# Optimization experiments

Hardware: AMD Instinct MI355X
Metric: run time of the kernel (lower is better)

The kernel has to match this reference:

```python
import jax, jax.numpy as jnp
import numpy as np

N, K, DIN = 2, 2048, 1024
H, DOUT = 16, 64


def setup_inputs() -> dict:
    key = jax.random.key(0)
    ks = jax.random.split(key, 12)
    c_qk = float(np.sqrt(6.0 / (DIN + DOUT)))  # per-head q/k init scale
    c_v = c_qk  # dim_q == dim_v == DOUT here
    u = lambda k, shape, c: jax.random.uniform(k, shape, jnp.float32, -c, c)
    inp = {
        "query": jax.random.normal(ks[0], (N, K, DIN), jnp.float32),
        "key": jax.random.normal(ks[1], (N, K, DIN), jnp.float32),
        "value": jax.random.normal(ks[2], (N, K, DIN), jnp.float32),
        "mask": jax.random.randint(ks[3], (N, K, K), 0, 2) > 0,  # bool (N,K,K)
        # stacked per-head projection weights: (H, DIN, DOUT), biases (H, DOUT)
        "Wq": u(ks[4], (H, DIN, DOUT), c_qk),
        "bq": u(ks[5], (H, DOUT), c_qk),
        "Wk": u(ks[6], (H, DIN, DOUT), c_qk),
        "bk": u(ks[7], (H, DOUT), c_qk),
        "Wv": u(ks[8], (H, DIN, DOUT), c_v),
        "bv": u(ks[9], (H, DOUT), c_v),
        # output projection: (H*DOUT, DIN)
        "Wp": u(ks[10], (H * DOUT, DIN), c_qk),
        "bp": u(ks[11], (DIN,), c_qk),
    }
    return inp


def reference(query, key, value, mask, Wq, bq, Wk, bk, Wv, bv, Wp, bp):
    # Per-head projections, batched over heads: (N,K,DIN) x (H,DIN,DOUT) -> (N,H,K,DOUT)
    q = jnp.einsum("nkm,hmd->nhkd", query, Wq) + bq[None, :, None, :]
    k = jnp.einsum("nkm,hmd->nhkd", key, Wk) + bk[None, :, None, :]
    v = jnp.einsum("nkm,hmd->nhkd", value, Wv) + bv[None, :, None, :]
    # scaled dot-product scores: (N,H,K,K), scaled by sqrt(per-head dim)
    scores = jnp.einsum("nhkd,nhld->nhkl", q, k) / jnp.sqrt(jnp.asarray(DOUT, q.dtype))
    scores = jnp.where(mask[:, None, :, :], jnp.asarray(-1e9, scores.dtype), scores)
    w = jax.nn.softmax(scores, axis=-1)
    y = jnp.einsum("nhkl,nhld->nhkd", w, v)  # (N,H,K,DOUT)
    # concat heads along feature dim (head order matches torch cat over head list)
    y = jnp.transpose(y, (0, 2, 1, 3)).reshape(N, K, H * DOUT)
    return y @ Wp + bp
```

## Files before the change

### kernel.cpp

```cpp
#include <hip/hip_runtime.h>
#include <hip/hip_bf16.h>
#include <stdint.h>

typedef __attribute__((ext_vector_type(8))) __bf16 bf16x8;
typedef __attribute__((ext_vector_type(2))) __bf16 bf16x2;
typedef __attribute__((ext_vector_type(4))) float floatx4;

#define NB 2
#define SEQ 2048
#define DIN 1024
#define NH 16
#define DH 64
#define DMODEL 1024
#define BQ 128
#define BK 64
#define PAD 72
#define QSCALE 0.18033688011112042f

__device__ __forceinline__ float bf2f(unsigned short u) {
    return __uint_as_float(((unsigned)u) << 16);
}
__device__ __forceinline__ unsigned short f2bf(float f) {
    unsigned u = __float_as_uint(f);
    unsigned r = (u + 0x7FFFu + ((u >> 16) & 1u)) >> 16;
    return (unsigned short)r;
}
__device__ __forceinline__ float ldin(const void* p, size_t idx, int isbf) {
    return isbf ? bf2f(((const unsigned short*)p)[idx]) : ((const float*)p)[idx];
}

__device__ __forceinline__ void gl_lds16(const void* g, void* l) {
    __builtin_amdgcn_global_load_lds(
        reinterpret_cast<__attribute__((address_space(1))) unsigned int*>(
            reinterpret_cast<uintptr_t>(g)),
        reinterpret_cast<__attribute__((address_space(3))) unsigned int*>(
            reinterpret_cast<uintptr_t>(l)),
        16, 0, 0);
}

__device__ __forceinline__ int wave_is_bf16(const void* p) {
    unsigned short u = ((const unsigned short*)p)[2 * (threadIdx.x & 63)];
    int e = (u >> 7) & 0xFF;
    int sane = (u == 0 || (e > 100 && e < 140)) ? 1 : 0;
    return __popcll(__ballot(sane)) >= 32;
}
__device__ __forceinline__ int wave_mask_is_int(const void* p) {
    int v = ((const int*)p)[threadIdx.x & 63];
    int zo = (v == 0 || v == 1) ? 1 : 0;
    return __popcll(__ballot(zo)) >= 48;
}

__global__ __launch_bounds__(256) void prep(
    const void* __restrict__ q, const void* __restrict__ k, const void* __restrict__ v,
    const void* __restrict__ mask,
    const void* __restrict__ wq, const void* __restrict__ wk,
    const void* __restrict__ wv, const void* __restrict__ wp,
    unsigned short* __restrict__ a0, unsigned short* __restrict__ a1,
    unsigned short* __restrict__ a2,
    unsigned short* __restrict__ t0, unsigned short* __restrict__ t1,
    unsigned short* __restrict__ t2, unsigned short* __restrict__ t3,
    unsigned int* __restrict__ mbits)
{
    __shared__ float xls[64][68];
    const int b = blockIdx.x;
    const int tid = threadIdx.x;
    if (b < 12288) {
        int z = b >> 12, blk = b & 4095;
        const void* src = (z == 0) ? q : (z == 1) ? k : v;
        unsigned short* dst = (z == 0) ? a0 : (z == 1) ? a1 : a2;
        int isbf = wave_is_bf16(src);
        size_t i = ((size_t)blk * 256 + tid) * 4;
        if (isbf) {
            *(ushort4*)&dst[i] = *(const ushort4*)((const unsigned short*)src + i);
        } else {
            float4 f = *(const float4*)((const float*)src + i);
            ushort4 o;
            o.x = f2bf(f.x); o.y = f2bf(f.y); o.z = f2bf(f.z); o.w = f2bf(f.w);
            *(ushort4*)&dst[i] = o;
        }
    } else if (b < 13312) {
        int blk = b - 12288;
        int w = blk * 256 + tid;
        int is_int = wave_mask_is_int(mask);
        unsigned bits = 0;
        if (is_int) {
            const int4* p = (const int4*)mask + (size_t)w * 8;
#pragma unroll
            for (int g = 0; g < 8; ++g) {
                int4 vv = p[g];
                bits |= (unsigned)(vv.x != 0) << (g * 4 + 0);
                bits |= (unsigned)(vv.y != 0) << (g * 4 + 1);
                bits |= (unsigned)(vv.z != 0) << (g * 4 + 2);
                bits |= (unsigned)(vv.w != 0) << (g * 4 + 3);
            }
        } else {
            const uint4* p = (const uint4*)mask + (size_t)w * 2;
#pragma unroll
            for (int g = 0; g < 2; ++g) {
                uint4 vv = p[g];
                unsigned ws4[4] = {vv.x, vv.y, vv.z, vv.w};
#pragma unroll
                for (int c = 0; c < 4; ++c)
#pragma unroll
                    for (int bb = 0; bb < 4; ++bb)
                        bits |= (unsigned)(((ws4[c] >> (8 * bb)) & 0xFFu) != 0)
                                << (g * 16 + c * 4 + bb);
            }
        }
        mbits[w] = bits;
    } else {
        int zb = b - 13312;
        int z = zb >> 8, t = zb & 255;
        const void* src = (z == 0) ? wq : (z == 1) ? wk : (z == 2) ? wv : wp;
        unsigned short* dst = (z == 0) ? t0 : (z == 1) ? t1 : (z == 2) ? t2 : t3;
        int isbf = wave_is_bf16(src);
        int r = tid >> 2, cs = (tid & 3) * 16;
        if (z < 3) {
            int h = t >> 4, m0 = (t & 15) * 64;
#pragma unroll
            for (int j = 0; j < 16; ++j)
                xls[r][cs + j] = ldin(src, (size_t)h * 65536 + (size_t)(m0 + r) * 64 + cs + j, isbf);
            __syncthreads();
            int d2 = tid >> 2, ms = (tid & 3) * 16;
            size_t orow = (size_t)(h * 64 + d2) * 1024 + m0 + ms;
#pragma unroll
            for (int g = 0; g < 4; ++g) {
                ushort4 o;
                o.x = f2bf(xls[ms + g * 4 + 0][d2]);
                o.y = f2bf(xls[ms + g * 4 + 1][d2]);
                o.z = f2bf(xls[ms + g * 4 + 2][d2]);
                o.w = f2bf(xls[ms + g * 4 + 3][d2]);
                *(ushort4*)&dst[orow + g * 4] = o;
            }
        } else {
            int m0 = (t >> 4) * 64, c0 = (t & 15) * 64;
#pragma unroll
            for (int j = 0; j < 16; ++j)
                xls[r][cs + j] = ldin(src, (size_t)(m0 + r) * 1024 + c0 + cs + j, isbf);
            __syncthreads();
            int d2 = tid >> 2, ms = (tid & 3) * 16;
            size_t orow = (size_t)(c0 + d2) * 1024 + m0 + ms;
#pragma unroll
            for (int g = 0; g < 4; ++g) {
                ushort4 o;
                o.x = f2bf(xls[ms + g * 4 + 0][d2]);
                o.y = f2bf(xls[ms + g * 4 + 1][d2]);
                o.z = f2bf(xls[ms + g * 4 + 2][d2]);
                o.w = f2bf(xls[ms + g * 4 + 3][d2]);
                *(ushort4*)&dst[orow + g * 4] = o;
            }
        }
    }
}

__global__ __launch_bounds__(256) void gemm_mfma(
    const unsigned short* __restrict__ A0, const unsigned short* __restrict__ A1,
    const unsigned short* __restrict__ A2,
    const unsigned short* __restrict__ B0, const unsigned short* __restrict__ B1,
    const unsigned short* __restrict__ B2,
    const void* __restrict__ bias0, const void* __restrict__ bias1,
    const void* __restrict__ bias2,
    void* __restrict__ C0, void* __restrict__ C1, void* __restrict__ C2,
    int mode0)
{
    const int z = blockIdx.z;
    const unsigned short* A  = (z == 0) ? A0 : (z == 1) ? A1 : A2;
    const unsigned short* BT = (z == 0) ? B0 : (z == 1) ? B1 : B2;
    const void* bias = (z == 0) ? bias0 : (z == 1) ? bias1 : bias2;
    void* C = (z == 0) ? C0 : (z == 1) ? C1 : C2;
    const int mode = mode0 + z;
    const int isbf = wave_is_bf16(bias);
    const float scl = (mode == 0) ? QSCALE : 1.0f;

    const int n0  = blockIdx.x * 128;
    const int m0g = blockIdx.y * 128;
    const int tid = threadIdx.x;
    const int wave = tid >> 6, lane = tid & 63;
    const int l16 = lane & 15, quad = lane >> 4;
    const int wm = wave & 1, wn = wave >> 1;

    __shared__ __align__(16) unsigned short smem[17408];
    unsigned short* As = smem;
    unsigned short* Bs = smem + 8192;

    floatx4 acc[4][4];
#pragma unroll
    for (int mt = 0; mt < 4; ++mt)
#pragma unroll
        for (int nt = 0; nt < 4; ++nt) acc[mt][nt] = floatx4{0.f, 0.f, 0.f, 0.f};

    const int lrow8 = lane >> 3;
    const int lseg  = (lane & 7) * 8;

    for (int kk = 0; kk < 1024; kk += 64) {
#pragma unroll
        for (int j = 0; j < 4; ++j) {
            int row0 = wave * 8 + j * 32;
            gl_lds16(&A[(size_t)(m0g + row0 + lrow8) * 1024 + kk + lseg], &As[row0 * 64]);
            gl_lds16(&BT[(size_t)(n0 + row0 + lrow8) * 1024 + kk + lseg], &Bs[row0 * 64]);
        }
        __syncthreads();
#pragma unroll
        for (int ks = 0; ks < 2; ++ks) {
            bf16x8 af[4], bf[4];
#pragma unroll
            for (int mt = 0; mt < 4; ++mt)
                af[mt] = *(const bf16x8*)&As[(wm * 64 + mt * 16 + l16) * 64 + ks * 32 + quad * 8];
#pragma unroll
            for (int nt = 0; nt < 4; ++nt)
                bf[nt] = *(const bf16x8*)&Bs[(wn * 64 + nt * 16 + l16) * 64 + ks * 32 + quad * 8];
#pragma unroll
            for (int mt = 0; mt < 4; ++mt)
#pragma unroll
                for (int nt = 0; nt < 4; ++nt)
                    acc[mt][nt] = __builtin_amdgcn_mfma_f32_16x16x32_bf16(af[mt], bf[nt], acc[mt][nt], 0, 0, 0);
        }
        __syncthreads();
    }

    float bv4[4];
#pragma unroll
    for (int nt = 0; nt < 4; ++nt)
        bv4[nt] = ldin(bias, n0 + wn * 64 + nt * 16 + l16, isbf);

    if (mode <= 1) {
        unsigned short* O = (unsigned short*)C;
#pragma unroll
        for (int mt = 0; mt < 4; ++mt)
#pragma unroll
            for (int reg = 0; reg < 4; ++reg) {
                int row = m0g + wm * 64 + mt * 16 + quad * 4 + reg;
                int nb = row >> 11, kq = row & (SEQ - 1);
#pragma unroll
                for (int nt = 0; nt < 4; ++nt) {
                    int c = n0 + wn * 64 + nt * 16 + l16;
                    int h = c >> 6, d = c & 63;
                    O[(((size_t)nb * NH + h) * SEQ + kq) * DH + d] =
                        f2bf((acc[mt][nt][reg] + bv4[nt]) * scl);
                }
            }
    } else if (mode == 2) {
#pragma unroll
        for (int mt = 0; mt < 4; ++mt)
#pragma unroll
            for (int nt = 0; nt < 4; ++nt)
#pragma unroll
                for (int reg = 0; reg < 4; ++reg) {
                    int m_l = wm * 64 + mt * 16 + quad * 4 + reg;
                    int c_l = wn * 64 + nt * 16 + l16;
                    smem[c_l * 136 + m_l] = f2bf(acc[mt][nt][reg] + bv4[nt]);
                }
        __syncthreads();
        unsigned short* O = (unsigned short*)C;
        int nb = m0g >> 11;
        int kq0 = m0g & (SEQ - 1);
#pragma unroll
        for (int j = 0; j < 8; ++j) {
            int i = tid + j * 256;
            int c_l = i >> 4, m8 = (i & 15) * 8;
            int cg = n0 + c_l, h = cg >> 6, d = cg & 63;
            *(bf16x8*)&O[(((size_t)nb * NH + h) * DH + d) * SEQ + kq0 + m8] =
                *(const bf16x8*)&smem[c_l * 136 + m8];
        }
    } else {
        unsigned short* Ob = (unsigned short*)C;
        float* Of = (float*)C;
#pragma unroll
        for (int mt = 0; mt < 4; ++mt)
#pragma unroll
            for (int reg = 0; reg < 4; ++reg) {
                int row = m0g + wm * 64 + mt * 16 + quad * 4 + reg;
#pragma unroll
                for (int nt = 0; nt < 4; ++nt) {
                    int c = n0 + wn * 64 + nt * 16 + l16;
                    float v = acc[mt][nt][reg] + bv4[nt];
                    if (isbf) Ob[(size_t)row * DMODEL + c] = f2bf(v);
                    else      Of[(size_t)row * DMODEL + c] = v;
                }
            }
    }
}

__global__ __launch_bounds__(256, 2) void attn_mfma(
    const unsigned short* __restrict__ qws, const unsigned short* __restrict__ kws,
    const unsigned short* __restrict__ vtws, const unsigned int* __restrict__ mbits,
    unsigned short* __restrict__ yws)
{
    const int linear = blockIdx.x + (blockIdx.y << 4) + (blockIdx.z << 8);
    const int xcd = linear & 7, loc = linear >> 3;
    const int hn  = (xcd << 2) + (loc >> 4);
    const int qt  = loc & 15;
    const int h   = hn & 15;
    const int n   = hn >> 4;

    const int tid  = threadIdx.x;
    const int wave = tid >> 6;
    const int lane = tid & 63;
    const int l16  = lane & 15;
    const int quad = lane >> 4;

    __shared__ __align__(16) unsigned short Ks[2][BK * DH];
    __shared__ __align__(16) unsigned short VTs[2][DH * BK];
    __shared__ __align__(16) unsigned short Ps[4][32 * PAD];

    const size_t base_nh = ((size_t)n * NH + h) * SEQ * DH;
    const size_t base_vt = ((size_t)n * NH + h) * DH * SEQ;
    const int q0 = qt * BQ;

    const unsigned int* mr0;
    const unsigned int* mr1;
    bf16x8 af[2][2];
    {
        int qr0 = q0 + wave * 32 + l16;
        int qr1 = qr0 + 16;
        mr0 = mbits + ((size_t)n * SEQ + qr0) * (SEQ / 32);
        mr1 = mbits + ((size_t)n * SEQ + qr1) * (SEQ / 32);
        const unsigned short* qp0 = qws + base_nh + (size_t)qr0 * DH + quad * 8;
        const unsigned short* qp1 = qws + base_nh + (size_t)qr1 * DH + quad * 8;
        af[0][0] = *(const bf16x8*)qp0;
        af[0][1] = *(const bf16x8*)(qp0 + 32);
        af[1][0] = *(const bf16x8*)qp1;
        af[1][1] = *(const bf16x8*)(qp1 + 32);
    }

    const int srow8  = lane >> 3;
    const int schunk = ((lane & 7) ^ srow8) * 8;
    const int swz = l16 & 7;
    int koff[2], voff[2];
#pragma unroll
    for (int ks = 0; ks < 2; ++ks) {
        koff[ks] = l16 * DH + (((ks * 4 + quad) ^ swz) * 8);
        voff[ks] = l16 * BK + (((ks * 4 + quad) ^ swz) * 8);
    }

    bf16x8 vones;
#pragma unroll
    for (int j = 0; j < 8; ++j) vones[j] = (__bf16)1.0f;

#pragma unroll
    for (int j = 0; j < 2; ++j) {
        int rl = wave * 16 + j * 8;
        gl_lds16(&kws[base_nh + (size_t)(rl + srow8) * DH + schunk], &Ks[0][rl * DH]);
        gl_lds16(&vtws[base_vt + (size_t)(rl + srow8) * SEQ + schunk], &VTs[0][rl * BK]);
    }

    floatx4 O[2][4];
#pragma unroll
    for (int g = 0; g < 2; ++g)
#pragma unroll
        for (int dt = 0; dt < 4; ++dt) O[g][dt] = floatx4{0.f, 0.f, 0.f, 0.f};
    floatx4 Lacc[2];
    Lacc[0] = floatx4{0.f, 0.f, 0.f, 0.f};
    Lacc[1] = floatx4{0.f, 0.f, 0.f, 0.f};

    __syncthreads();

    for (int it = 0; it < SEQ / BK; ++it) {
        const int cur = it & 1, nxt = cur ^ 1;
        const bool has_next = (it + 1) < (SEQ / BK);
        const int j0 = it * BK;
        const int j0n = j0 + BK;

        if (has_next) {
#pragma unroll
            for (int j = 0; j < 2; ++j) {
                int rl = wave * 16 + j * 8;
                gl_lds16(&kws[base_nh + (size_t)(j0n + rl + srow8) * DH + schunk], &Ks[nxt][rl * DH]);
                gl_lds16(&vtws[base_vt + (size_t)(rl + srow8) * SEQ + j0n + schunk], &VTs[nxt][rl * BK]);
            }
        }

        uint2 mwA = *(const uint2*)&mr0[j0 >> 5];
        uint2 mwB = *(const uint2*)&mr1[j0 >> 5];

        bf16x8 bfK[4][2];
#pragma unroll
        for (int nt = 0; nt < 4; ++nt)
#pragma unroll
            for (int ks = 0; ks < 2; ++ks)
                bfK[nt][ks] = *(const bf16x8*)&Ks[cur][nt * 16 * DH + koff[ks]];

        float St[2][4][4];
#pragma unroll
        for (int nt = 0; nt < 4; ++nt) {
#pragma unroll
            for (int g = 0; g < 2; ++g) {
                floatx4 c = {0.f, 0.f, 0.f, 0.f};
                c = __builtin_amdgcn_mfma_f32_16x16x32_bf16(bfK[nt][0], af[g][0], c, 0, 0, 0);
                c = __builtin_amdgcn_mfma_f32_16x16x32_bf16(bfK[nt][1], af[g][1], c, 0, 0, 0);
                St[g][nt][0] = c[0]; St[g][nt][1] = c[1];
                St[g][nt][2] = c[2]; St[g][nt][3] = c[3];
            }
        }

#pragma unroll
        for (int g = 0; g < 2; ++g) {
            uint2 mw = g ? mwB : mwA;
#pragma unroll
            for (int nt = 0; nt < 4; ++nt) {
                unsigned w = (nt & 2) ? mw.y : mw.x;
                int bb = (nt & 1) * 16 + quad * 4;
                float p[4];
#pragma unroll
                for (int r = 0; r < 4; ++r) {
                    float e = __builtin_amdgcn_exp2f(St[g][nt][r]);
                    p[r] = ((w >> (bb + r)) & 1u) ? 0.f : e;
                }
                bf16x2 e01, e23;
                e01[0] = (__bf16)p[0]; e01[1] = (__bf16)p[1];
                e23[0] = (__bf16)p[2]; e23[1] = (__bf16)p[3];
                uint2 pk;
                pk.x = *(unsigned*)&e01;
                pk.y = *(unsigned*)&e23;
                *(uint2*)&Ps[wave][(g * 16 + l16) * PAD + nt * 16 + quad * 4] = pk;
            }
        }

        bf16x8 pa[2][2], vb[4][2];
#pragma unroll
        for (int g = 0; g < 2; ++g)
#pragma unroll
            for (int ks = 0; ks < 2; ++ks)
                pa[g][ks] = *(const bf16x8*)&Ps[wave][(g * 16 + l16) * PAD + ks * 32 + quad * 8];
#pragma unroll
        for (int dt = 0; dt < 4; ++dt)
#pragma unroll
            for (int ks = 0; ks < 2; ++ks)
                vb[dt][ks] = *(const bf16x8*)&VTs[cur][dt * 16 * BK + voff[ks]];

        Lacc[0] = __builtin_amdgcn_mfma_f32_16x16x32_bf16(pa[0][0], vones, Lacc[0], 0, 0, 0);
        Lacc[1] = __builtin_amdgcn_mfma_f32_16x16x32_bf16(pa[1][0], vones, Lacc[1], 0, 0, 0);
        Lacc[0] = __builtin_amdgcn_mfma_f32_16x16x32_bf16(pa[0][1], vones, Lacc[0], 0, 0, 0);
        Lacc[1] = __builtin_amdgcn_mfma_f32_16x16x32_bf16(pa[1][1], vones, Lacc[1], 0, 0, 0);
#pragma unroll
        for (int dt = 0; dt < 4; ++dt) {
#pragma unroll
            for (int g = 0; g < 2; ++g) {
                O[g][dt] = __builtin_amdgcn_mfma_f32_16x16x32_bf16(pa[g][0], vb[dt][0], O[g][dt], 0, 0, 0);
                O[g][dt] = __builtin_amdgcn_mfma_f32_16x16x32_bf16(pa[g][1], vb[dt][1], O[g][dt], 0, 0, 0);
            }
        }

        __syncthreads();
    }

#pragma unroll
    for (int g = 0; g < 2; ++g)
#pragma unroll
        for (int r = 0; r < 4; ++r) {
            float lr = Lacc[g][r];
            float inv = (lr > 0.f) ? 1.f / lr : 0.f;
            int row = q0 + wave * 32 + g * 16 + quad * 4 + r;
#pragma unroll
            for (int dt = 0; dt < 4; ++dt) {
                int col = h * DH + dt * 16 + l16;
                yws[((size_t)n * SEQ + row) * DMODEL + col] = f2bf(O[g][dt][r] * inv);
            }
        }
}

extern "C" void kernel_launch(void* const* d_in, const int* in_sizes, int n_in,
                              void* d_out, int out_size, void* d_ws, size_t ws_size,
                              hipStream_t stream) {
    const void* query = d_in[0];
    const void* key_  = d_in[1];
    const void* value = d_in[2];
    const void* mask  = d_in[3];
    const void* Wq = d_in[4];
    const void* bq = d_in[5];
    const void* Wk = d_in[6];
    const void* bk = d_in[7];
    const void* Wv = d_in[8];
    const void* bv = d_in[9];
    const void* Wp = d_in[10];
    const void* bp = d_in[11];

    const size_t per = (size_t)NB * NH * SEQ * DH;
    unsigned short* us = (unsigned short*)d_ws;
    unsigned short* qws  = us;
    unsigned short* kws  = us + per;
    unsigned short* vtws = us + 2 * per;
    unsigned short* abf0 = us + 3 * per;
    unsigned short* abf1 = us + 4 * per;
    unsigned short* abf2 = us + 5 * per;
    unsigned short* wt0  = us + 6 * per;
    unsigned short* wt1  = wt0 + 1048576;
    unsigned short* wt2  = wt1 + 1048576;
    unsigned short* wt3  = wt2 + 1048576;
    unsigned int* mbits  = (unsigned int*)(wt3 + 1048576);
    unsigned short* yws = abf0;

    prep<<<dim3(14336), 256, 0, stream>>>(query, key_, value, mask,
                                          Wq, Wk, Wv, Wp,
                                          abf0, abf1, abf2,
                                          wt0, wt1, wt2, wt3, mbits);
    gemm_mfma<<<dim3(8, 32, 3), 256, 0, stream>>>(abf0, abf1, abf2, wt0, wt1, wt2,
                                                  bq, bk, bv, qws, kws, vtws, 0);
    attn_mfma<<<dim3(SEQ / BQ, NH, NB), 256, 0, stream>>>(qws, kws, vtws, mbits, yws);
    gemm_mfma<<<dim3(8, 32, 1), 256, 0, stream>>>(yws, yws, yws, wt3, wt3, wt3,
                                                  bp, bp, bp, d_out, d_out, d_out, 3);
}
```

Measured before the change: 287.8 us.

## Triple-buffer K/V tiles with partial vmcnt waits and MFMA priority boosts

Replaces the double-buffered K/V LDS pipeline with a three-stage ring that prefetches two tiles ahead, and prefetches the mask words two iterations ahead. The full __syncthreads is replaced by an explicit s_waitcnt vmcnt(6) plus s_barrier, so the current tile's loads must land while the newest prefetch stays in flight. s_setprio is raised around the MFMA blocks to favour matrix issue across waves. This adds LDS usage, which may affect occupancy at 2 blocks/CU, and relies on the hand-counted vmcnt being correct.

```diff
diff --git a/kernel.cpp b/kernel.cpp
--- a/kernel.cpp
+++ b/kernel.cpp
@@ -299,8 +299,8 @@
     const int l16  = lane & 15;
     const int quad = lane >> 4;
 
-    __shared__ __align__(16) unsigned short Ks[2][BK * DH];
-    __shared__ __align__(16) unsigned short VTs[2][DH * BK];
+    __shared__ __align__(16) unsigned short Ks[3][BK * DH];
+    __shared__ __align__(16) unsigned short VTs[3][DH * BK];
     __shared__ __align__(16) unsigned short Ps[4][32 * PAD];
 
     const size_t base_nh = ((size_t)n * NH + h) * SEQ * DH;
@@ -337,12 +337,15 @@
 #pragma unroll
     for (int j = 0; j < 8; ++j) vones[j] = (__bf16)1.0f;
 
-#pragma unroll
-    for (int j = 0; j < 2; ++j) {
-        int rl = wave * 16 + j * 8;
-        gl_lds16(&kws[base_nh + (size_t)(rl + srow8) * DH + schunk], &Ks[0][rl * DH]);
-        gl_lds16(&vtws[base_vt + (size_t)(rl + srow8) * SEQ + schunk], &VTs[0][rl * BK]);
-    }
+    auto stage = [&](int b, int t) {
+        int j0t = t * BK;
+#pragma unroll
+        for (int j = 0; j < 2; ++j) {
+            int rl = wave * 16 + j * 8;
+            gl_lds16(&kws[base_nh + (size_t)(j0t + rl + srow8) * DH + schunk], &Ks[b][rl * DH]);
+            gl_lds16(&vtws[base_vt + (size_t)(rl + srow8) * SEQ + j0t + schunk], &VTs[b][rl * BK]);
+        }
+    };
 
     floatx4 O[2][4];
 #pragma unroll
@@ -353,25 +356,24 @@
     Lacc[0] = floatx4{0.f, 0.f, 0.f, 0.f};
     Lacc[1] = floatx4{0.f, 0.f, 0.f, 0.f};
 
-    __syncthreads();
-
+    stage(0, 0);
+    stage(1, 1);
+    uint2 mwA_c = *(const uint2*)&mr0[0];
+    uint2 mwB_c = *(const uint2*)&mr1[0];
+    uint2 mwA_n = *(const uint2*)&mr0[2];
+    uint2 mwB_n = *(const uint2*)&mr1[2];
+    asm volatile("s_waitcnt vmcnt(0)" ::: "memory");
+    __builtin_amdgcn_s_barrier();
+
+    int cur = 0;
     for (int it = 0; it < SEQ / BK; ++it) {
-        const int cur = it & 1, nxt = cur ^ 1;
-        const bool has_next = (it + 1) < (SEQ / BK);
-        const int j0 = it * BK;
-        const int j0n = j0 + BK;
-
-        if (has_next) {
-#pragma unroll
-            for (int j = 0; j < 2; ++j) {
-                int rl = wave * 16 + j * 8;
-                gl_lds16(&kws[base_nh + (size_t)(j0n + rl + srow8) * DH + schunk], &Ks[nxt][rl * DH]);
-                gl_lds16(&vtws[base_vt + (size_t)(rl + srow8) * SEQ + j0n + schunk], &VTs[nxt][rl * BK]);
-            }
-        }
-
-        uint2 mwA = *(const uint2*)&mr0[j0 >> 5];
-        uint2 mwB = *(const uint2*)&mr1[j0 >> 5];
+        uint2 nA = {0, 0}, nB = {0, 0};
+        if (it + 2 < SEQ / BK) {
+            int b2 = cur + 2; b2 = (b2 >= 3) ? b2 - 3 : b2;
+            stage(b2, it + 2);
+            nA = *(const uint2*)&mr0[(it + 2) * 2];
+            nB = *(const uint2*)&mr1[(it + 2) * 2];
+        }
 
         bf16x8 bfK[4][2];
 #pragma unroll
@@ -381,6 +383,7 @@
                 bfK[nt][ks] = *(const bf16x8*)&Ks[cur][nt * 16 * DH + koff[ks]];
 
         float St[2][4][4];
+        __builtin_amdgcn_s_setprio(1);
 #pragma unroll
         for (int nt = 0; nt < 4; ++nt) {
 #pragma unroll
@@ -392,10 +395,11 @@
                 St[g][nt][2] = c[2]; St[g][nt][3] = c[3];
             }
         }
+        __builtin_amdgcn_s_setprio(0);
 
 #pragma unroll
         for (int g = 0; g < 2; ++g) {
-            uint2 mw = g ? mwB : mwA;
+            uint2 mw = g ? mwB_c : mwA_c;
 #pragma unroll
             for (int nt = 0; nt < 4; ++nt) {
                 unsigned w = (nt & 2) ? mw.y : mw.x;
@@ -428,6 +432,7 @@
             for (int ks = 0; ks < 2; ++ks)
                 vb[dt][ks] = *(const bf16x8*)&VTs[cur][dt * 16 * BK + voff[ks]];
 
+        __builtin_amdgcn_s_setprio(1);
         Lacc[0] = __builtin_amdgcn_mfma_f32_16x16x32_bf16(pa[0][0], vones, Lacc[0], 0, 0, 0);
         Lacc[1] = __builtin_amdgcn_mfma_f32_16x16x32_bf16(pa[1][0], vones, Lacc[1], 0, 0, 0);
         Lacc[0] = __builtin_amdgcn_mfma_f32_16x16x32_bf16(pa[0][1], vones, Lacc[0], 0, 0, 0);
@@ -440,8 +445,19 @@
                 O[g][dt] = __builtin_amdgcn_mfma_f32_16x16x32_bf16(pa[g][1], vb[dt][1], O[g][dt], 0, 0, 0);
             }
         }
-
-        __syncthreads();
+        __builtin_amdgcn_s_setprio(0);
+
+        if (it + 1 < SEQ / BK) {
+            if (it < SEQ / BK - 2)
+                asm volatile("s_waitcnt vmcnt(6)" ::: "memory");
+            else
+                asm volatile("s_waitcnt vmcnt(0)" ::: "memory");
+            __builtin_amdgcn_s_barrier();
+        }
+
+        cur = (cur == 2) ? 0 : cur + 1;
+        mwA_c = mwA_n; mwB_c = mwB_n;
+        mwA_n = nA;    mwB_n = nB;
     }
 
 #pragma unroll
```

New measurement: 287.2 us. No clear change (-0.2%).
